# Performance work log

Hardware: AMD Instinct MI355X
Metric: run time of the kernel (lower is better)

The kernel has to match this reference:

```python
import jax, jax.numpy as jnp
import numpy as np

D_IN = 512
D = 1024      # new_embed_dim
H = 16        # num_heads
HD = D // H   # head_dim


def setup_inputs() -> dict:
    key = jax.random.key(0)
    ks = jax.random.split(key, 16)
    g = lambda k, shape, fan: jax.random.normal(k, shape, jnp.float32) / np.sqrt(fan)
    return {
        "x1": jax.random.normal(ks[0], (16, 1, D_IN), jnp.float32),
        "x2": jax.random.normal(ks[1], (16, 4096, D_IN), jnp.float32),
        "x3": jax.random.normal(ks[2], (16, 4096, D_IN), jnp.float32),
        # embedding1 (for x1) and embedding2 (used for BOTH x2 and x3, per source)
        "We1": g(ks[3], (D_IN, D), D_IN), "be1": jnp.zeros((D,), jnp.float32),
        "We2": g(ks[4], (D_IN, D), D_IN), "be2": jnp.zeros((D,), jnp.float32),
        "Wq": g(ks[5], (D, D), D), "bq": jnp.zeros((D,), jnp.float32),
        "Wk": g(ks[6], (D, D), D), "bk": jnp.zeros((D,), jnp.float32),
        "Wv": g(ks[7], (D, D), D), "bv": jnp.zeros((D,), jnp.float32),
        "Wo": g(ks[8], (D, D), D), "bo": jnp.zeros((D,), jnp.float32),
    }


def reference(x1, x2, x3, We1, be1, We2, be2, Wq, bq, Wk, bk, Wv, bv, Wo, bo):
    B = x1.shape[0]
    # embeddings (x3 intentionally uses embedding2's weights, matching source)
    x1e = x1 @ We1 + be1                      # [B,1,D]
    x2e = x2 @ We2 + be2                      # [B,S,D]
    x3e = x3 @ We2 + be2                      # [B,S,D]
    q = (x1e @ Wq + bq).reshape(B, -1, H, HD).transpose(0, 2, 1, 3)  # [B,H,1,HD]
    k = (x2e @ Wk + bk).reshape(B, -1, H, HD).transpose(0, 2, 1, 3)  # [B,H,S,HD]
    v = (x3e @ Wv + bv).reshape(B, -1, H, HD).transpose(0, 2, 1, 3)  # [B,H,S,HD]
    scale = jnp.asarray(np.sqrt(HD), q.dtype)
    attn = jax.nn.softmax(jnp.einsum("bhqd,bhkd->bhqk", q, k) / scale, axis=-1)
    # dropout is identity at inference (keras training=False default)
    av = jnp.einsum("bhqk,bhkd->bhqd", attn, v)          # [B,H,1,HD]
    av = av.transpose(0, 2, 1, 3).reshape(B, -1, D)      # [B,1,D]
    out = av @ Wo + bo                                   # [B,1,D]
    return jnp.squeeze(out, axis=1)                      # [B,D]
```

## Files before the change

kernel.cpp:

```cpp
#include <hip/hip_runtime.h>


#define DIN 512
#define DD  1024
#define NH  16
#define HD  64
#define BB  16
#define SS  4096

__device__ __forceinline__ int wave_id() {
    return __builtin_amdgcn_readfirstlane((int)(threadIdx.x >> 6));
}

__global__ __launch_bounds__(256) void k_transpose(const float* __restrict__ in,
                                                   float* __restrict__ out,
                                                   int R, int C) {
    __shared__ float tl[32][33];
    const int tx = threadIdx.x & 31, ty = threadIdx.x >> 5;
    const int c0 = blockIdx.x * 32, r0 = blockIdx.y * 32;
#pragma unroll
    for (int k = 0; k < 4; ++k) {
        int r = r0 + ty + k * 8;
        tl[ty + k * 8][tx] = in[(size_t)r * C + c0 + tx];
    }
    __syncthreads();
#pragma unroll
    for (int k = 0; k < 4; ++k) {
        int c = c0 + ty + k * 8;
        out[(size_t)c * R + r0 + tx] = tl[tx][ty + k * 8];
    }
}

__global__ __launch_bounds__(256) void k_init(const float* __restrict__ be1,
                                              const float* __restrict__ bq,
                                              const float* __restrict__ bv,
                                              const float* __restrict__ bo,
                                              float* __restrict__ x1e,
                                              float* __restrict__ qb,
                                              float* __restrict__ av,
                                              float* __restrict__ out) {
    const int b = blockIdx.x;
#pragma unroll
    for (int k = 0; k < 4; ++k) {
        const int c = k * 256 + threadIdx.x;
        x1e[(size_t)b * DD + c] = be1[c];
        qb[(size_t)b * DD + c]  = bq[c];
        av[(size_t)b * DD + c]  = bv[c];
        out[(size_t)b * DD + c] = bo[c];
    }
}

template <int K, int N, int KS, bool HASB>
__global__ __launch_bounds__(256) void k_bmv2(const float* __restrict__ in,
                                              const float* __restrict__ W,
                                              const float* __restrict__ bias,
                                              float* __restrict__ out) {
    const int l = threadIdx.x & 63;
    const int c = blockIdx.x * 64 + l;
    const int wv = wave_id();
    constexpr int KCH = K / KS;
    constexpr int SUB = KCH / 4;
    const float* inb = in + (size_t)blockIdx.y * 16 * K;
    float acc[16];
#pragma unroll
    for (int r = 0; r < 16; ++r) acc[r] = 0.f;
    const int i0 = blockIdx.z * KCH + wv * SUB;
#pragma unroll 4
    for (int i = i0; i < i0 + SUB; ++i) {
        const float wval = W[(size_t)i * N + c];
#pragma unroll
        for (int r = 0; r < 16; ++r) acc[r] += inb[(size_t)r * K + i] * wval;
    }
    __shared__ float red[4][16][64];
#pragma unroll
    for (int r = 0; r < 16; ++r) red[wv][r][l] = acc[r];
    __syncthreads();
#pragma unroll
    for (int k = 0; k < 4; ++k) {
        const int r = wv + k * 4;
        float v = red[0][r][l] + red[1][r][l] + red[2][r][l] + red[3][r][l];
        float* dst = out + ((size_t)blockIdx.y * 16 + r) * N + c;
        if (KS == 1) {
            if (HASB) v += bias[c];
            *dst = v;
        } else {
            atomicAdd(dst, v);
        }
    }
}

__global__ __launch_bounds__(256) void k_u2(const float* __restrict__ q,
                                            const float* __restrict__ WkT,
                                            float* __restrict__ u) {
    const int h = blockIdx.y;
    const int l = threadIdx.x & 63;
    const int c = blockIdx.x * 64 + l;
    const int wv = wave_id();
    float acc[16];
#pragma unroll
    for (int bb = 0; bb < 16; ++bb) acc[bb] = 0.f;
#pragma unroll 4
    for (int dk = 0; dk < 16; ++dk) {
        const int d = wv * 16 + dk;
        const float wval = WkT[(size_t)(h * HD + d) * DD + c];
#pragma unroll
        for (int bb = 0; bb < 16; ++bb)
            acc[bb] += q[(size_t)bb * DD + h * HD + d] * wval;
    }
    __shared__ float red[4][16][64];
#pragma unroll
    for (int bb = 0; bb < 16; ++bb) red[wv][bb][l] = acc[bb];
    __syncthreads();
#pragma unroll
    for (int k = 0; k < 4; ++k) {
        const int bb = wv + k * 4;
        float v = red[0][bb][l] + red[1][bb][l] + red[2][bb][l] + red[3][bb][l];
        u[((size_t)bb * NH + h) * DD + c] = v;
    }
}

__global__ __launch_bounds__(256) void k_scores(const float* __restrict__ x2,
                                                const float* __restrict__ w,
                                                float* __restrict__ sc) {
    __shared__ float4 tile[64 * 32];
    const int b = blockIdx.y;
    const int s0 = blockIdx.x * 64;
    const int l = threadIdx.x & 63;
    const int h0 = wave_id() * 4;
    const float4* x2f = (const float4*)x2 + ((size_t)b * SS + s0) * (DIN / 4);
    float a0 = 0.f, a1 = 0.f, a2 = 0.f, a3 = 0.f;
#pragma unroll
    for (int kt = 0; kt < 4; ++kt) {
#pragma unroll
        for (int k = 0; k < 8; ++k) {
            const int j = threadIdx.x + k * 256;
            const int row = j >> 5, c4 = j & 31;
            tile[row * 32 + (c4 ^ (row & 7))] = x2f[row * (DIN / 4) + kt * 32 + c4];
        }
        __syncthreads();
        const float4* wp = (const float4*)(w + ((size_t)b * NH + h0) * DIN + kt * 128);
#pragma unroll 8
        for (int c4 = 0; c4 < 32; ++c4) {
            const float4 x = tile[l * 32 + (c4 ^ (l & 7))];
            const float4 q0 = wp[c4];
            const float4 q1 = wp[128 + c4];
            const float4 q2 = wp[256 + c4];
            const float4 q3 = wp[384 + c4];
            a0 += x.x * q0.x + x.y * q0.y + x.z * q0.z + x.w * q0.w;
            a1 += x.x * q1.x + x.y * q1.y + x.z * q1.z + x.w * q1.w;
            a2 += x.x * q2.x + x.y * q2.y + x.z * q2.z + x.w * q2.w;
            a3 += x.x * q3.x + x.y * q3.y + x.z * q3.z + x.w * q3.w;
        }
        __syncthreads();
    }
    const size_t base = ((size_t)b * NH + h0) * SS + s0 + l;
    sc[base + 0 * SS] = a0;
    sc[base + 1 * SS] = a1;
    sc[base + 2 * SS] = a2;
    sc[base + 3 * SS] = a3;
}

__global__ __launch_bounds__(256) void k_softmax(float* __restrict__ sc) {
    float4* row = (float4*)(sc + (size_t)blockIdx.x * SS);
    float4 v[4];
    float m = -1e30f;
#pragma unroll
    for (int j = 0; j < 4; ++j) {
        v[j] = row[threadIdx.x + j * 256];
        m = fmaxf(m, fmaxf(fmaxf(v[j].x, v[j].y), fmaxf(v[j].z, v[j].w)));
    }
    __shared__ float red[256];
    red[threadIdx.x] = m;
    __syncthreads();
    for (int s = 128; s > 0; s >>= 1) {
        if (threadIdx.x < (unsigned)s)
            red[threadIdx.x] = fmaxf(red[threadIdx.x], red[threadIdx.x + s]);
        __syncthreads();
    }
    m = red[0];
    __syncthreads();
    float sum = 0.f;
#pragma unroll
    for (int j = 0; j < 4; ++j) {
        v[j].x = expf((v[j].x - m) * 0.125f);
        v[j].y = expf((v[j].y - m) * 0.125f);
        v[j].z = expf((v[j].z - m) * 0.125f);
        v[j].w = expf((v[j].w - m) * 0.125f);
        sum += v[j].x + v[j].y + v[j].z + v[j].w;
    }
    red[threadIdx.x] = sum;
    __syncthreads();
    for (int s = 128; s > 0; s >>= 1) {
        if (threadIdx.x < (unsigned)s) red[threadIdx.x] += red[threadIdx.x + s];
        __syncthreads();
    }
    const float inv = 1.f / red[0];
#pragma unroll
    for (int j = 0; j < 4; ++j) {
        v[j].x *= inv; v[j].y *= inv; v[j].z *= inv; v[j].w *= inv;
        row[threadIdx.x + j * 256] = v[j];
    }
}

__global__ __launch_bounds__(256) void k_gpart(const float* __restrict__ x3,
                                               const float* __restrict__ a,
                                               float* __restrict__ gp,
                                               int schunk, int nch) {
    const int b = blockIdx.y, ch = blockIdx.x;
    const int wv = wave_id();
    const int l = threadIdx.x & 63;
    const int sub = schunk >> 2;
    const int sbeg = ch * schunk + wv * sub;
    const float* ar = a + (size_t)b * NH * SS;
    float acc[16][8];
#pragma unroll
    for (int h = 0; h < 16; ++h)
#pragma unroll
        for (int j = 0; j < 8; ++j) acc[h][j] = 0.f;

    for (int s = sbeg; s < sbeg + sub; ++s) {
        const float4* xr = (const float4*)(x3 + ((size_t)b * SS + s) * DIN);
        const float4 xa = xr[l];
        const float4 xb = xr[l + 64];
        const float xv[8] = {xa.x, xa.y, xa.z, xa.w, xb.x, xb.y, xb.z, xb.w};
#pragma unroll
        for (int h = 0; h < 16; ++h) {
            const float wh = ar[h * SS + s];
#pragma unroll
            for (int j = 0; j < 8; ++j) acc[h][j] += wh * xv[j];
        }
    }

    __shared__ float red[4][2048];
    for (int hg = 0; hg < 4; ++hg) {
        __syncthreads();
#pragma unroll
        for (int hh = 0; hh < 4; ++hh) {
            float* dst = &red[wv][hh * 512];
            const int hs = hg * 4 + hh;
            *(float4*)(dst + l * 4) =
                make_float4(acc[hs][0], acc[hs][1], acc[hs][2], acc[hs][3]);
            *(float4*)(dst + 256 + l * 4) =
                make_float4(acc[hs][4], acc[hs][5], acc[hs][6], acc[hs][7]);
        }
        __syncthreads();
        const int idx = threadIdx.x * 8;
        float o[8];
#pragma unroll
        for (int j = 0; j < 8; ++j)
            o[j] = red[0][idx + j] + red[1][idx + j] + red[2][idx + j] + red[3][idx + j];
        const int hh = idx >> 9;
        const int i = idx & 511;
        float* dst = gp + (((size_t)(b * nch + ch) * NH) + hg * 4 + hh) * DIN + i;
        *(float4*)dst = make_float4(o[0], o[1], o[2], o[3]);
        *(float4*)(dst + 4) = make_float4(o[4], o[5], o[6], o[7]);
    }
}

__global__ __launch_bounds__(256) void k_greduce(const float* __restrict__ gp, int nch,
                                                 float* __restrict__ g) {
    const int pair = blockIdx.x;
    const int b = pair >> 4, h = pair & 15;
#pragma unroll
    for (int kk = 0; kk < 2; ++kk) {
        const int i = kk * 256 + threadIdx.x;
        float acc = 0.f;
        for (int ch = 0; ch < nch; ++ch)
            acc += gp[((size_t)(b * nch + ch) * NH + h) * DIN + i];
        g[(size_t)pair * DIN + i] = acc;
    }
}

__global__ __launch_bounds__(256) void k_av_at(const float* __restrict__ G2,
                                               const float* __restrict__ Wv,
                                               float* __restrict__ av) {
    const int h = blockIdx.x;
    const int l = threadIdx.x & 63;
    const int wv = wave_id();
    const int c0 = blockIdx.y * 128 + wv * 32;
    float acc[16];
#pragma unroll
    for (int bb = 0; bb < 16; ++bb) acc[bb] = 0.f;
#pragma unroll 4
    for (int c = c0; c < c0 + 32; ++c) {
        const float wval = Wv[(size_t)c * DD + h * HD + l];
#pragma unroll
        for (int bb = 0; bb < 16; ++bb)
            acc[bb] += G2[((size_t)bb * NH + h) * DD + c] * wval;
    }
    __shared__ float red[4][16][64];
#pragma unroll
    for (int bb = 0; bb < 16; ++bb) red[wv][bb][l] = acc[bb];
    __syncthreads();
#pragma unroll
    for (int k = 0; k < 4; ++k) {
        const int bb = wv + k * 4;
        float v = red[0][bb][l] + red[1][bb][l] + red[2][bb][l] + red[3][bb][l];
        atomicAdd(&av[(size_t)bb * DD + h * HD + l], v);
    }
}

extern "C" void kernel_launch(void* const* d_in, const int* in_sizes, int n_in,
                              void* d_out, int out_size, void* d_ws, size_t ws_size,
                              hipStream_t stream) {
    const float* x1  = (const float*)d_in[0];
    const float* x2  = (const float*)d_in[1];
    const float* x3  = (const float*)d_in[2];
    const float* We1 = (const float*)d_in[3];
    const float* be1 = (const float*)d_in[4];
    const float* We2 = (const float*)d_in[5];
    const float* be2 = (const float*)d_in[6];
    const float* Wq  = (const float*)d_in[7];
    const float* bq  = (const float*)d_in[8];
    const float* Wk  = (const float*)d_in[9];
    const float* bk  = (const float*)d_in[10];
    const float* Wv  = (const float*)d_in[11];
    const float* bv  = (const float*)d_in[12];
    const float* Wo  = (const float*)d_in[13];
    const float* bo  = (const float*)d_in[14];
    (void)bk;
    float* out = (float*)d_out;

    char* ws = (char*)d_ws;
    size_t off = 0;
    auto alloc = [&](size_t bytes) -> void* {
        void* p = ws + off;
        off = (off + bytes + 255) & ~(size_t)255;
        return p;
    };
    float* We2t = (float*)alloc((size_t)DD * DIN * 4);
    float* WkT  = (float*)alloc((size_t)DD * DD * 4);
    float* x1e  = (float*)alloc((size_t)BB * DD * 4);
    float* qb   = (float*)alloc((size_t)BB * DD * 4);
    float* u    = (float*)alloc((size_t)BB * NH * DD * 4);
    float* wv_  = (float*)alloc((size_t)BB * NH * DIN * 4);
    float* sc   = (float*)alloc((size_t)BB * NH * SS * 4);
    float* g    = (float*)alloc((size_t)BB * NH * DIN * 4);
    float* G2   = (float*)alloc((size_t)BB * NH * DD * 4);
    float* av   = (float*)alloc((size_t)BB * DD * 4);

    const size_t per_chunk = (size_t)BB * NH * DIN * 4;
    int nch = 32;
    while (nch > 8 && off + (size_t)nch * per_chunk > ws_size) nch >>= 1;
    float* gp = (float*)alloc((size_t)nch * per_chunk);
    const int schunk = SS / nch;

    k_transpose<<<dim3(DD / 32, DIN / 32), 256, 0, stream>>>(We2, We2t, DIN, DD);
    k_transpose<<<dim3(DD / 32, DD / 32), 256, 0, stream>>>(Wk, WkT, DD, DD);
    k_init<<<BB, 256, 0, stream>>>(be1, bq, bv, bo, x1e, qb, av, out);
    k_bmv2<DIN, DD, 8, false><<<dim3(DD / 64, 1, 8), 256, 0, stream>>>(x1, We1, nullptr, x1e);
    k_bmv2<DD, DD, 8, false><<<dim3(DD / 64, 1, 8), 256, 0, stream>>>(x1e, Wq, nullptr, qb);
    k_u2<<<dim3(DD / 64, NH), 256, 0, stream>>>(qb, WkT, u);
    k_bmv2<DD, DIN, 1, false><<<dim3(DIN / 64, BB * NH / 16, 1), 256, 0, stream>>>(u, We2t, nullptr, wv_);
    k_scores<<<dim3(SS / 64, BB), 256, 0, stream>>>(x2, wv_, sc);
    k_softmax<<<BB * NH, 256, 0, stream>>>(sc);
    k_gpart<<<dim3(nch, BB), 256, 0, stream>>>(x3, sc, gp, schunk, nch);
    k_greduce<<<BB * NH, 256, 0, stream>>>(gp, nch, g);
    k_bmv2<DIN, DD, 1, true><<<dim3(DD / 64, BB * NH / 16, 1), 256, 0, stream>>>(g, We2, be2, G2);
    k_av_at<<<dim3(NH, 8), 256, 0, stream>>>(G2, Wv, av);
    k_bmv2<DD, DD, 8, false><<<dim3(DD / 64, 1, 8), 256, 0, stream>>>(av, Wo, nullptr, out);
}
```

Before: 462.6 us.

## Fuse prep kernels, double-buffer score tiles, replace gpart reduction with atomics

Merges the two weight transposes and the bias init into one launch, which now also zeroes g. k_scores moves to a double-buffered shared tile with register prefetch of the next K-slice, removing one barrier per iteration. k_gpart accumulates its per-chunk partials straight into g with atomicAdd, so the gp buffer and the k_greduce launch go away. This cuts launches and global traffic but adds atomic contention and makes the summation order nondeterministic.

```diff
diff --git a/kernel.cpp b/kernel.cpp
--- a/kernel.cpp
+++ b/kernel.cpp
@@ -12,41 +12,53 @@
     return __builtin_amdgcn_readfirstlane((int)(threadIdx.x >> 6));
 }
 
-__global__ __launch_bounds__(256) void k_transpose(const float* __restrict__ in,
-                                                   float* __restrict__ out,
-                                                   int R, int C) {
+__device__ __forceinline__ void tile_transpose(const float* __restrict__ in,
+                                               float* __restrict__ out,
+                                               int R, int C, int rblk, int cblk) {
     __shared__ float tl[32][33];
     const int tx = threadIdx.x & 31, ty = threadIdx.x >> 5;
-    const int c0 = blockIdx.x * 32, r0 = blockIdx.y * 32;
-#pragma unroll
-    for (int k = 0; k < 4; ++k) {
-        int r = r0 + ty + k * 8;
-        tl[ty + k * 8][tx] = in[(size_t)r * C + c0 + tx];
-    }
-    __syncthreads();
-#pragma unroll
-    for (int k = 0; k < 4; ++k) {
-        int c = c0 + ty + k * 8;
-        out[(size_t)c * R + r0 + tx] = tl[tx][ty + k * 8];
-    }
-}
-
-__global__ __launch_bounds__(256) void k_init(const float* __restrict__ be1,
+    const int c0 = cblk * 32, r0 = rblk * 32;
+#pragma unroll
+    for (int k = 0; k < 4; ++k)
+        tl[ty + k * 8][tx] = in[(size_t)(r0 + ty + k * 8) * C + c0 + tx];
+    __syncthreads();
+#pragma unroll
+    for (int k = 0; k < 4; ++k)
+        out[(size_t)(c0 + ty + k * 8) * R + r0 + tx] = tl[tx][ty + k * 8];
+}
+
+__global__ __launch_bounds__(256) void k_prep(const float* __restrict__ We2,
+                                              const float* __restrict__ Wk,
+                                              const float* __restrict__ be1,
                                               const float* __restrict__ bq,
                                               const float* __restrict__ bv,
                                               const float* __restrict__ bo,
+                                              float* __restrict__ We2t,
+                                              float* __restrict__ WkT,
                                               float* __restrict__ x1e,
                                               float* __restrict__ qb,
                                               float* __restrict__ av,
-                                              float* __restrict__ out) {
-    const int b = blockIdx.x;
-#pragma unroll
-    for (int k = 0; k < 4; ++k) {
-        const int c = k * 256 + threadIdx.x;
-        x1e[(size_t)b * DD + c] = be1[c];
-        qb[(size_t)b * DD + c]  = bq[c];
-        av[(size_t)b * DD + c]  = bv[c];
-        out[(size_t)b * DD + c] = bo[c];
+                                              float* __restrict__ out,
+                                              float* __restrict__ g) {
+    const int bx = blockIdx.x;
+    if (bx < 512) {
+        tile_transpose(We2, We2t, DIN, DD, bx >> 5, bx & 31);
+    } else if (bx < 1536) {
+        const int lb = bx - 512;
+        tile_transpose(Wk, WkT, DD, DD, lb >> 5, lb & 31);
+    } else {
+        const int b = bx - 1536;
+#pragma unroll
+        for (int k = 0; k < 4; ++k) {
+            const int c = k * 256 + threadIdx.x;
+            x1e[(size_t)b * DD + c] = be1[c];
+            qb[(size_t)b * DD + c]  = bq[c];
+            av[(size_t)b * DD + c]  = bv[c];
+            out[(size_t)b * DD + c] = bo[c];
+        }
+#pragma unroll
+        for (int k = 0; k < 32; ++k)
+            g[(size_t)b * 8192 + k * 256 + threadIdx.x] = 0.f;
     }
 }
 
@@ -122,36 +134,50 @@
 __global__ __launch_bounds__(256) void k_scores(const float* __restrict__ x2,
                                                 const float* __restrict__ w,
                                                 float* __restrict__ sc) {
-    __shared__ float4 tile[64 * 32];
+    __shared__ float4 tile[2][64 * 16];
     const int b = blockIdx.y;
     const int s0 = blockIdx.x * 64;
     const int l = threadIdx.x & 63;
     const int h0 = wave_id() * 4;
     const float4* x2f = (const float4*)x2 + ((size_t)b * SS + s0) * (DIN / 4);
+    const float4* wp = (const float4*)(w + ((size_t)b * NH + h0) * DIN);
+
+    float4 pf[4];
+#pragma unroll
+    for (int k = 0; k < 4; ++k) {
+        const int idx = threadIdx.x + k * 256;
+        pf[k] = x2f[(idx >> 4) * (DIN / 4) + (idx & 15)];
+    }
     float a0 = 0.f, a1 = 0.f, a2 = 0.f, a3 = 0.f;
 #pragma unroll
-    for (int kt = 0; kt < 4; ++kt) {
-#pragma unroll
-        for (int k = 0; k < 8; ++k) {
-            const int j = threadIdx.x + k * 256;
-            const int row = j >> 5, c4 = j & 31;
-            tile[row * 32 + (c4 ^ (row & 7))] = x2f[row * (DIN / 4) + kt * 32 + c4];
-        }
-        __syncthreads();
-        const float4* wp = (const float4*)(w + ((size_t)b * NH + h0) * DIN + kt * 128);
-#pragma unroll 8
-        for (int c4 = 0; c4 < 32; ++c4) {
-            const float4 x = tile[l * 32 + (c4 ^ (l & 7))];
-            const float4 q0 = wp[c4];
-            const float4 q1 = wp[128 + c4];
-            const float4 q2 = wp[256 + c4];
-            const float4 q3 = wp[384 + c4];
+    for (int kt = 0; kt < 8; ++kt) {
+        float4* buf = tile[kt & 1];
+#pragma unroll
+        for (int k = 0; k < 4; ++k) {
+            const int idx = threadIdx.x + k * 256;
+            const int row = idx >> 4, c4 = idx & 15;
+            buf[row * 16 + (c4 ^ (row & 7))] = pf[k];
+        }
+        __syncthreads();
+        if (kt < 7) {
+#pragma unroll
+            for (int k = 0; k < 4; ++k) {
+                const int idx = threadIdx.x + k * 256;
+                pf[k] = x2f[(idx >> 4) * (DIN / 4) + (kt + 1) * 16 + (idx & 15)];
+            }
+        }
+#pragma unroll
+        for (int c4 = 0; c4 < 16; ++c4) {
+            const float4 x = buf[l * 16 + (c4 ^ (l & 7))];
+            const float4 q0 = wp[kt * 16 + c4];
+            const float4 q1 = wp[128 + kt * 16 + c4];
+            const float4 q2 = wp[256 + kt * 16 + c4];
+            const float4 q3 = wp[384 + kt * 16 + c4];
             a0 += x.x * q0.x + x.y * q0.y + x.z * q0.z + x.w * q0.w;
             a1 += x.x * q1.x + x.y * q1.y + x.z * q1.z + x.w * q1.w;
             a2 += x.x * q2.x + x.y * q2.y + x.z * q2.z + x.w * q2.w;
             a3 += x.x * q3.x + x.y * q3.y + x.z * q3.z + x.w * q3.w;
         }
-        __syncthreads();
     }
     const size_t base = ((size_t)b * NH + h0) * SS + s0 + l;
     sc[base + 0 * SS] = a0;
@@ -204,8 +230,8 @@
 
 __global__ __launch_bounds__(256) void k_gpart(const float* __restrict__ x3,
                                                const float* __restrict__ a,
-                                               float* __restrict__ gp,
-                                               int schunk, int nch) {
+                                               float* __restrict__ g,
+                                               int schunk) {
     const int b = blockIdx.y, ch = blockIdx.x;
     const int wv = wave_id();
     const int l = threadIdx.x & 63;
@@ -218,6 +244,7 @@
 #pragma unroll
         for (int j = 0; j < 8; ++j) acc[h][j] = 0.f;
 
+#pragma unroll 2
     for (int s = sbeg; s < sbeg + sub; ++s) {
         const float4* xr = (const float4*)(x3 + ((size_t)b * SS + s) * DIN);
         const float4 xa = xr[l];
@@ -245,29 +272,15 @@
         }
         __syncthreads();
         const int idx = threadIdx.x * 8;
-        float o[8];
-#pragma unroll
-        for (int j = 0; j < 8; ++j)
-            o[j] = red[0][idx + j] + red[1][idx + j] + red[2][idx + j] + red[3][idx + j];
         const int hh = idx >> 9;
         const int i = idx & 511;
-        float* dst = gp + (((size_t)(b * nch + ch) * NH) + hg * 4 + hh) * DIN + i;
-        *(float4*)dst = make_float4(o[0], o[1], o[2], o[3]);
-        *(float4*)(dst + 4) = make_float4(o[4], o[5], o[6], o[7]);
-    }
-}
-
-__global__ __launch_bounds__(256) void k_greduce(const float* __restrict__ gp, int nch,
-                                                 float* __restrict__ g) {
-    const int pair = blockIdx.x;
-    const int b = pair >> 4, h = pair & 15;
-#pragma unroll
-    for (int kk = 0; kk < 2; ++kk) {
-        const int i = kk * 256 + threadIdx.x;
-        float acc = 0.f;
-        for (int ch = 0; ch < nch; ++ch)
-            acc += gp[((size_t)(b * nch + ch) * NH + h) * DIN + i];
-        g[(size_t)pair * DIN + i] = acc;
+        float* dst = g + ((size_t)b * NH + hg * 4 + hh) * DIN + i;
+#pragma unroll
+        for (int j = 0; j < 8; ++j) {
+            const float o =
+                red[0][idx + j] + red[1][idx + j] + red[2][idx + j] + red[3][idx + j];
+            atomicAdd(dst + j, o);
+        }
     }
 }
 
@@ -339,23 +352,18 @@
     float* G2   = (float*)alloc((size_t)BB * NH * DD * 4);
     float* av   = (float*)alloc((size_t)BB * DD * 4);
 
-    const size_t per_chunk = (size_t)BB * NH * DIN * 4;
-    int nch = 32;
-    while (nch > 8 && off + (size_t)nch * per_chunk > ws_size) nch >>= 1;
-    float* gp = (float*)alloc((size_t)nch * per_chunk);
+    const int nch = 32;
     const int schunk = SS / nch;
 
-    k_transpose<<<dim3(DD / 32, DIN / 32), 256, 0, stream>>>(We2, We2t, DIN, DD);
-    k_transpose<<<dim3(DD / 32, DD / 32), 256, 0, stream>>>(Wk, WkT, DD, DD);
-    k_init<<<BB, 256, 0, stream>>>(be1, bq, bv, bo, x1e, qb, av, out);
+    k_prep<<<1552, 256, 0, stream>>>(We2, Wk, be1, bq, bv, bo,
+                                     We2t, WkT, x1e, qb, av, out, g);
     k_bmv2<DIN, DD, 8, false><<<dim3(DD / 64, 1, 8), 256, 0, stream>>>(x1, We1, nullptr, x1e);
     k_bmv2<DD, DD, 8, false><<<dim3(DD / 64, 1, 8), 256, 0, stream>>>(x1e, Wq, nullptr, qb);
     k_u2<<<dim3(DD / 64, NH), 256, 0, stream>>>(qb, WkT, u);
     k_bmv2<DD, DIN, 1, false><<<dim3(DIN / 64, BB * NH / 16, 1), 256, 0, stream>>>(u, We2t, nullptr, wv_);
     k_scores<<<dim3(SS / 64, BB), 256, 0, stream>>>(x2, wv_, sc);
     k_softmax<<<BB * NH, 256, 0, stream>>>(sc);
-    k_gpart<<<dim3(nch, BB), 256, 0, stream>>>(x3, sc, gp, schunk, nch);
-    k_greduce<<<BB * NH, 256, 0, stream>>>(gp, nch, g);
+    k_gpart<<<dim3(nch, BB), 256, 0, stream>>>(x3, sc, g, schunk);
     k_bmv2<DIN, DD, 1, true><<<dim3(DD / 64, BB * NH / 16, 1), 256, 0, stream>>>(g, We2, be2, G2);
     k_av_at<<<dim3(NH, 8), 256, 0, stream>>>(G2, Wv, av);
     k_bmv2<DD, DD, 8, false><<<dim3(DD / 64, 1, 8), 256, 0, stream>>>(av, Wo, nullptr, out);
```

After: 741.2 us. 1.6x slower.
